# Optimization experiments

Hardware: AMD Instinct MI355X
Metric: run time of the kernel (lower is better)

The kernel has to match this reference:

```python
import math
import jax, jax.numpy as jnp
import numpy as np

NEG = -1.0e10  # matches LARGE_NUMBER padding in the original
K_SUBSET = 8
N_SAMPLES = 2


def log_conv(aL, aR, K):
    """Log-space convolution of two count distributions, truncated to counts 0..K-1.
    aL, aR: [..., K] log-values; returns c[m] = logsumexp_j aL[j] + aR[m-j]."""
    jj = jnp.arange(K)[:, None]
    mm = jnp.arange(K)[None, :]
    idx = mm - jj  # [K(j), K(m)]
    valid = idx >= 0
    aRg = aR[..., jnp.clip(idx, 0, K - 1)]  # [..., K, K]
    t = aL[..., :, None] + jnp.where(valid, aRg, NEG)
    return jax.nn.logsumexp(t, axis=-2)


def up_pass(theta, k):
    """theta: [B, N] logits (N power of two). Returns list of per-level log-ESP
    tables, levels[l]: [B, N/2^l, k+1]; levels[-1][:,0,j] = log e_j(exp theta)."""
    B, N = theta.shape
    K = k + 1
    leaf = jnp.full((B, N, K), NEG, theta.dtype)
    leaf = leaf.at[..., 0].set(0.0).at[..., 1].set(theta)
    levels = [leaf]
    a = leaf
    while a.shape[1] > 1:
        a = log_conv(a[:, 0::2], a[:, 1::2], K)
        levels.append(a)
    return levels


def down_marginals(levels, theta, k):
    """Exact inclusion marginals P(x_i=1 | sum=k) via tree forward-backward."""
    K = k + 1
    B = theta.shape[0]
    ext = jnp.full((B, 1, K), NEG, theta.dtype).at[..., 0].set(0.0)
    for lvl in range(len(levels) - 2, -1, -1):
        a = levels[lvl]
        aL, aR = a[:, 0::2], a[:, 1::2]
        extL = log_conv(ext, aR, K)  # ESP of everything outside left subtree
        extR = log_conv(ext, aL, K)
        ext = jnp.stack([extL, extR], axis=2).reshape(B, a.shape[1], K)
    logZ = levels[-1][:, 0, k]  # log e_k over all items
    # P(x_i=1) = exp(theta_i) * e_{k-1}(others) / e_k(all)
    return jnp.exp(theta + ext[..., k - 1] - logZ[:, None])


def sample_counts(levels, k, n_samples, key):
    """Top-down exact sampling of k-subsets; returns leaf counts [S, B, N] in {0,1}."""
    K = k + 1
    B = levels[0].shape[0]
    counts = jnp.full((n_samples, B, 1), k, jnp.int32)
    jj = jnp.arange(K)
    for lvl in range(len(levels) - 2, -1, -1):
        a = levels[lvl]
        aL, aR = a[:, 0::2], a[:, 1::2]
        n = aL.shape[1]
        idx = counts[..., None] - jj  # desired right-count, [S,B,n,K]
        valid = idx >= 0
        aRg = jnp.take_along_axis(
            jnp.broadcast_to(aR[None], (n_samples, B, n, K)),
            jnp.clip(idx, 0, k), axis=-1)
        logits = aL[None] + jnp.where(valid, aRg, NEG)
        key, sub = jax.random.split(key)
        g = jax.random.gumbel(sub, logits.shape, logits.dtype)
        cL = jnp.argmax(logits + g, axis=-1).astype(jnp.int32)
        cR = counts - cL
        counts = jnp.stack([cL, cR], axis=-1).reshape(n_samples, B, 2 * n)
    return counts


def setup_inputs() -> dict:
    key = jax.random.key(0)
    scores = jax.random.normal(key, (8192, 32, 8), dtype=jnp.float32)
    return {"scores": scores}


def reference(scores):
    nnodes, choices, ensemble = scores.shape
    k = min(K_SUBSET, choices)
    flat = jnp.transpose(scores, (0, 2, 1)).reshape(nnodes * ensemble, choices)
    N = 2 ** math.ceil(math.log2(choices))
    if N > choices:
        flat = jnp.concatenate(
            [flat, jnp.full((flat.shape[0], N - choices), NEG, flat.dtype)], axis=1)
    levels = up_pass(flat, k)
    marg_flat = down_marginals(levels, flat, k)[:, :choices]  # [B, choices]
    marginals = jnp.transpose(
        marg_flat.reshape(nnodes, ensemble, choices), (0, 2, 1))  # [nnodes, choices, ensemble]
    counts = sample_counts(levels, k, N_SAMPLES, jax.random.key(42))
    counts = counts[:, :, :choices].astype(scores.dtype)
    samples = jnp.transpose(
        counts.reshape(N_SAMPLES, nnodes, ensemble, choices), (0, 1, 3, 2))
    # straight-through: hard samples forward, marginal gradients backward
    samples = jax.lax.stop_gradient(samples - marginals[None]) + marginals[None]
    return samples, marginals
```

## Files before the change

### kernel.cpp

```cpp
#include <hip/hip_runtime.h>
#include <stdint.h>


__host__ __device__ __forceinline__ void tf2x32(uint32_t k0, uint32_t k1,
                                                uint32_t x0, uint32_t x1,
                                                uint32_t& y0, uint32_t& y1) {
  const uint32_t ks[3] = {k0, k1, k0 ^ k1 ^ 0x1BD11BDAu};
  x0 += ks[0]; x1 += ks[1];
  const int R0[4] = {13, 15, 26, 6};
  const int R1[4] = {17, 29, 16, 24};
#pragma unroll
  for (int i = 0; i < 5; ++i) {
    const int* R = (i & 1) ? R1 : R0;
#pragma unroll
    for (int rr = 0; rr < 4; ++rr) {
      x0 += x1;
      x1 = (x1 << R[rr]) | (x1 >> (32 - R[rr]));
      x1 ^= x0;
    }
    x0 += ks[(i + 1) % 3];
    x1 += ks[(i + 2) % 3] + (uint32_t)(i + 1);
  }
  y0 = x0; y1 = x1;
}

struct TFKeys { uint32_t v[10]; };

__device__ __forceinline__ float gumbel_draw(uint32_t sk0, uint32_t sk1,
                                             uint32_t f) {
  uint32_t y0, y1;
  tf2x32(sk0, sk1, 0u, f, y0, y1);
  uint32_t bits = y0 ^ y1;
  uint32_t fb = (bits >> 9) | 0x3f800000u;
  float u = __uint_as_float(fb) - 1.0f;
  const float tiny = 1.17549435e-38f;
  float rr = fmaxf(tiny, u + tiny);
  return -logf(-logf(rr));
}

template<bool FAST> __device__ __forceinline__ float expT(float x) {
  return FAST ? __expf(x) : expf(x);
}
template<bool FAST> __device__ __forceinline__ float logT(float x) {
  return FAST ? __logf(x) : logf(x);
}

template<int SIN, int SOUT, bool FAST>
__device__ __forceinline__ void conv_level(const float (&aL)[SIN],
                                           const float (&aR)[SIN],
                                           float (&o)[SOUT]) {
#pragma unroll
  for (int m = 1; m < SOUT; ++m) {
    const int jlo = (m - (SIN - 1) > 0) ? (m - (SIN - 1)) : 0;
    const int jhi = (m < SIN - 1) ? m : (SIN - 1);
    float t[SIN];
#pragma unroll
    for (int j = 0; j < SIN; ++j)
      if (j >= jlo && j <= jhi) t[j] = aL[j] + aR[m - j];
    float amax = t[jlo];
#pragma unroll
    for (int j = 0; j < SIN; ++j)
      if (j > jlo && j <= jhi) amax = fmaxf(amax, t[j]);
    float s = 0.0f;
#pragma unroll
    for (int j = 0; j < SIN; ++j)
      if (j >= jlo && j <= jhi) s += expT<FAST>(t[j] - amax);
    o[m] = logT<FAST>(s) + amax;
  }
}

template<int SSIB, int MLO, int MHI, bool FAST>
__device__ __forceinline__ void ext_level(const float (&ein)[8],
                                          const float* sib, float (&eo)[8]) {
#pragma unroll
  for (int m = MLO; m <= MHI; ++m) {
    const int jlo = (m - (SSIB - 1) > 0) ? (m - (SSIB - 1)) : 0;
    float t[8];
#pragma unroll
    for (int j = 0; j < 8; ++j)
      if (j >= jlo && j <= m) t[j] = ein[j] + sib[m - j];
    float amax = t[jlo];
#pragma unroll
    for (int j = 0; j < 8; ++j)
      if (j > jlo && j <= m) amax = fmaxf(amax, t[j]);
    float s = 0.0f;
#pragma unroll
    for (int j = 0; j < 8; ++j)
      if (j >= jlo && j <= m) s += expT<FAST>(t[j] - amax);
    eo[m] = logT<FAST>(s) + amax;
  }
}

#define ENT 144

__global__ __launch_bounds__(128, 2) void simple_sampler_kernel(
    const float* __restrict__ scores, float* __restrict__ out,
    int nnodes, TFKeys keys) {
  const int tid = threadIdx.x;
  const int w = tid >> 6;
  const int lane = tid & 63;
  const int p = lane & 1;
  const int r = lane >> 1;
  const int row = (blockIdx.x * 2 + w) * 32 + r;
  const int node = row >> 3, e = row & 7;
  const int B = nnodes * 8;

  __shared__ float lds[2 * ENT * 32];
  float* W = &lds[w * (ENT * 32)];
#define L(E) W[(E) * 32 + r]

  float th[16];
  const float* sc = scores + node * 256 + e + p * 128;
#pragma unroll
  for (int c = 0; c < 16; ++c) th[c] = sc[c * 8];
#pragma unroll
  for (int c = 0; c < 16; ++c) L(16 * p + c) = th[c];

  float l1r[8], th2r[8];
#pragma unroll
  for (int n1l = 0; n1l < 8; ++n1l) {
    float tL = th[2 * n1l], tR = th[2 * n1l + 1];
    float amax = fmaxf(tR, tL);
    float s = expf(tR - amax) + expf(tL - amax);
    l1r[n1l] = logf(s) + amax;
    th2r[n1l] = tL + tR;
    int n1 = 8 * p + n1l;
    L(32 + n1) = l1r[n1l];
    L(48 + n1) = th2r[n1l];
  }
  float l2r[4][5];
#pragma unroll
  for (int n2l = 0; n2l < 4; ++n2l) {
    float aL[3] = {0.0f, l1r[2 * n2l], th2r[2 * n2l]};
    float aR[3] = {0.0f, l1r[2 * n2l + 1], th2r[2 * n2l + 1]};
    float o5[5];
    conv_level<3, 5, false>(aL, aR, o5);
    l2r[n2l][0] = 0.0f;
    int n2 = 4 * p + n2l;
#pragma unroll
    for (int m = 1; m < 5; ++m) { l2r[n2l][m] = o5[m]; L(64 + n2 * 4 + m - 1) = o5[m]; }
  }
  float l3r[2][9];
#pragma unroll
  for (int n3l = 0; n3l < 2; ++n3l) {
    float o9[9];
    conv_level<5, 9, false>(l2r[2 * n3l], l2r[2 * n3l + 1], o9);
    l3r[n3l][0] = 0.0f;
    int n3 = 2 * p + n3l;
#pragma unroll
    for (int m = 1; m < 9; ++m) { l3r[n3l][m] = o9[m]; L(96 + n3 * 8 + m - 1) = o9[m]; }
  }
  {
    float o9[9];
    conv_level<9, 9, false>(l3r[0], l3r[1], o9);
#pragma unroll
    for (int m = 1; m < 9; ++m) L(128 + p * 8 + m - 1) = o9[m];
  }

  __builtin_amdgcn_wave_barrier();

  float A0[9], A1[9];
  A0[0] = 0.0f; A1[0] = 0.0f;
#pragma unroll
  for (int m = 1; m < 9; ++m) { A0[m] = L(128 + m - 1); A1[m] = L(136 + m - 1); }

  float logZ;
  {
    float t[9];
#pragma unroll
    for (int j = 0; j < 9; ++j) t[j] = A0[j] + A1[8 - j];
    float amax = t[0];
#pragma unroll
    for (int j = 1; j < 9; ++j) amax = fmaxf(amax, t[j]);
    float s = 0.0f;
#pragma unroll
    for (int j = 0; j < 9; ++j) s += __expf(t[j] - amax);
    logZ = __logf(s) + amax;
  }

  {
    float e4v[8];
    e4v[0] = 0.0f;
#pragma unroll
    for (int m = 1; m < 8; ++m) e4v[m] = p ? A0[m] : A1[m];
    float* mb = out + 2 * B * 32 + node * 256 + e;
#pragma unroll
    for (int n3l = 0; n3l < 2; ++n3l) {
      float e3[8];
      ext_level<9, 0, 7, true>(e4v, l3r[n3l ^ 1], e3);
#pragma unroll
      for (int c2 = 0; c2 < 2; ++c2) {
        const int n2l = 2 * n3l + c2;
        float e2v[8];
        ext_level<5, 4, 7, true>(e3, l2r[n2l ^ 1], e2v);
#pragma unroll
        for (int c1 = 0; c1 < 2; ++c1) {
          const int n1l = 2 * n2l + c1;
          float sib1[3] = {0.0f, l1r[n1l ^ 1], th2r[n1l ^ 1]};
          float e1m[8];
          ext_level<3, 6, 7, true>(e2v, sib1, e1m);
          const int colL = 16 * p + 2 * n1l;
          {
            float t6 = e1m[6] + th[2 * n1l + 1];
            float t7 = e1m[7];
            float amax = fmaxf(t6, t7);
            float s = __expf(t6 - amax) + __expf(t7 - amax);
            mb[colL * 8] = __expf((th[2 * n1l] + (__logf(s) + amax)) - logZ);
          }
          {
            float t6 = e1m[6] + th[2 * n1l];
            float t7 = e1m[7];
            float amax = fmaxf(t6, t7);
            float s = __expf(t6 - amax) + __expf(t7 - amax);
            mb[(colL + 1) * 8] = __expf((th[2 * n1l + 1] + (__logf(s) + amax)) - logZ);
          }
        }
      }
    }
  }

  const uint32_t t9 = (uint32_t)(p * B + row) * 9u;
  int c0, c1;
  {
    float best = 0.0f; int bj = 0;
#pragma unroll
    for (int j = 0; j < 9; ++j) {
      float g = gumbel_draw(keys.v[0], keys.v[1], t9 + (uint32_t)j);
      float v = (A0[j] + A1[8 - j]) + g;
      if (j == 0) { best = v; } else if (v > best) { best = v; bj = j; }
    }
    c0 = bj; c1 = 8 - bj;
  }
  int c1v[4];
  {
    const int n0 = c0 ? c0 + 1 : 0;
    const int n1c = c1 ? c1 + 1 : 0;
    const int tot = n0 + n1c;
    float b0 = -3.0e38f, b1 = -3.0e38f;
    int j0 = 0, j1 = 0;
    for (int t = 0; t < tot; ++t) {
      const bool is1 = (t >= n0);
      const int j = is1 ? (t - n0) : t;
      const int c = is1 ? c1 : c0;
      const int i = is1 ? 1 : 0;
      const int idx = c - j;
      float aL = (j == 0) ? 0.0f : L(96 + 16 * i + j - 1);
      float aR = (idx == 0) ? 0.0f : L(96 + 16 * i + 8 + idx - 1);
      float g = gumbel_draw(keys.v[2], keys.v[3],
                            2u * t9 + (uint32_t)(9 * i + j));
      float v = (aL + aR) + g;
      if (is1) { if (v > b1) { b1 = v; j1 = j; } }
      else     { if (v > b0) { b0 = v; j0 = j; } }
    }
    c1v[0] = j0; c1v[1] = c0 - j0; c1v[2] = j1; c1v[3] = c1 - j1;
  }
  uint32_t pk2 = 0;
  {
#pragma unroll
    for (int i = 0; i < 4; ++i) {
      int c = c1v[i];
      float best = -3.0e38f; int bj = 0;
#pragma unroll
      for (int j = 0; j < 5; ++j) {
        float g = gumbel_draw(keys.v[4], keys.v[5],
                              4u * t9 + (uint32_t)(i * 9 + j));
        int idx = c - j;
        int cl = min(max(idx, 1), 4);
        float ar = L(64 + (2 * i + 1) * 4 + cl - 1);
        float af = (idx == 0) ? 0.0f : ar;
        float aL = (j == 0) ? 0.0f : L(64 + (2 * i) * 4 + j - 1);
        float v = (aL + af) + g;
        if (idx >= 0 && idx <= 4 && v > best) { best = v; bj = j; }
      }
      pk2 |= ((uint32_t)bj << (8 * i)) | ((uint32_t)(c - bj) << (8 * i + 4));
    }
  }
  uint64_t pk64 = 0;
  {
    const uint32_t sk0 = keys.v[6], sk1 = keys.v[7];
    const uint32_t fb0 = 8u * t9;
#pragma unroll 2
    for (int i = 0; i < 8; ++i) {
      int c = (int)((pk2 >> (4 * i)) & 15u);
      float aL1 = L(32 + 2 * i), aL2 = L(48 + 2 * i);
      float arm1 = L(32 + 2 * i + 1), arm2 = L(48 + 2 * i + 1);
      uint32_t fb = fb0 + (uint32_t)(i * 9);
      float best = -3.0e38f; int bj = 0;
#pragma unroll
      for (int j = 0; j < 3; ++j) {
        float g = gumbel_draw(sk0, sk1, fb + (uint32_t)j);
        int idx = c - j;
        float af = (idx == 1) ? arm1 : ((idx == 2) ? arm2 : 0.0f);
        float aLj = (j == 0) ? 0.0f : ((j == 1) ? aL1 : aL2);
        float v = (aLj + af) + g;
        if (idx >= 0 && idx <= 2 && v > best) { best = v; bj = j; }
      }
      pk64 |= ((uint64_t)(uint32_t)bj << (8 * i)) |
              ((uint64_t)(uint32_t)(c - bj) << (8 * i + 4));
    }
  }
  {
    const uint32_t sk0 = keys.v[8], sk1 = keys.v[9];
    const uint32_t fb0 = 16u * t9;
    float* bs = out + p * (B * 32) + node * 256 + e;
    uint64_t lst = 0; int m4 = 0;
#pragma unroll
    for (int i = 0; i < 16; ++i) {
      int c = (int)((uint32_t)(pk64 >> (4 * i)) & 15u);
      if (c == 1) {
        lst |= ((uint64_t)(uint32_t)i) << (4 * m4);
        ++m4;
      } else {
        int bj = c >> 1;
        bs[16 * i] = (float)bj;
        bs[16 * i + 8] = (float)(c - bj);
      }
    }
    for (int t = 0; t < m4; ++t) {
      int i = (int)((lst >> (4 * t)) & 15u);
      float thL = L(2 * i);
      float thR = L(2 * i + 1);
      uint32_t fb = fb0 + (uint32_t)(i * 9);
      float g0 = gumbel_draw(sk0, sk1, fb);
      float g1 = gumbel_draw(sk0, sk1, fb + 1u);
      float v0 = thR + g0;
      float v1 = thL + g1;
      int bj = (v1 > v0) ? 1 : 0;
      bs[16 * i] = (float)bj;
      bs[16 * i + 8] = (float)(1 - bj);
    }
  }
#undef L
}

extern "C" void kernel_launch(void* const* d_in, const int* in_sizes, int n_in,
                              void* d_out, int out_size, void* d_ws, size_t ws_size,
                              hipStream_t stream) {
  const float* scores = (const float*)d_in[0];
  float* out = (float*)d_out;
  const int nnodes = in_sizes[0] / (32 * 8);
  const int B = nnodes * 8;

  TFKeys K;
  uint32_t k0 = 0u, k1 = 42u;
  for (int t = 0; t < 5; ++t) {
    uint32_t n0, n1, s0, s1;
    tf2x32(k0, k1, 0u, 0u, n0, n1);
    tf2x32(k0, k1, 0u, 1u, s0, s1);
    K.v[2 * t] = s0; K.v[2 * t + 1] = s1;
    k0 = n0; k1 = n1;
  }

  dim3 grid((unsigned)(B / 64)), block(128);
  hipLaunchKernelGGL(simple_sampler_kernel, grid, block, 0, stream,
                     scores, out, nnodes, K);
}
```

Before: 114.0 us.

## Split each row across four lanes to raise parallelism and occupancy

Each row is now handled by four lanes instead of two: every lane owns 8 of the 32 choices in the up pass, and the root level is spread across lanes through shared memory. The sampling descent is split by sample (p) and by half-tree (q), and the root choice is merged with a lane shuffle. Blocks grow to 256 threads with a padded shared table of stride 65, so each row gets twice the threads and fewer registers per thread. The cost is more shared-memory traffic and extra lane-to-lane exchange, and the root-level shared-memory sums use non-unrolled loops.

```diff
diff --git a/kernel.cpp b/kernel.cpp
--- a/kernel.cpp
+++ b/kernel.cpp
@@ -93,68 +93,87 @@
 
 #define ENT 144
 
-__global__ __launch_bounds__(128, 2) void simple_sampler_kernel(
+__global__ __launch_bounds__(256, 4) void simple_sampler_kernel(
     const float* __restrict__ scores, float* __restrict__ out,
     int nnodes, TFKeys keys) {
   const int tid = threadIdx.x;
   const int w = tid >> 6;
   const int lane = tid & 63;
-  const int p = lane & 1;
-  const int r = lane >> 1;
-  const int row = (blockIdx.x * 2 + w) * 32 + r;
+  const int sub = lane & 3;
+  const int q = sub & 1;
+  const int p = sub >> 1;
+  const int r = lane >> 2;
+  const int slot = w * 16 + r;
+  const int row = blockIdx.x * 64 + slot;
   const int node = row >> 3, e = row & 7;
   const int B = nnodes * 8;
-
-  __shared__ float lds[2 * ENT * 32];
-  float* W = &lds[w * (ENT * 32)];
-#define L(E) W[(E) * 32 + r]
-
-  float th[16];
-  const float* sc = scores + node * 256 + e + p * 128;
-#pragma unroll
-  for (int c = 0; c < 16; ++c) th[c] = sc[c * 8];
-#pragma unroll
-  for (int c = 0; c < 16; ++c) L(16 * p + c) = th[c];
-
-  float l1r[8], th2r[8];
-#pragma unroll
-  for (int n1l = 0; n1l < 8; ++n1l) {
-    float tL = th[2 * n1l], tR = th[2 * n1l + 1];
+  const int t = sub;
+
+  __shared__ float tab[ENT * 65];
+#define L(E) tab[(E) * 65 + slot]
+
+  float th[8];
+  const float* sc = scores + node * 256 + e + t * 64;
+#pragma unroll
+  for (int c = 0; c < 8; ++c) th[c] = sc[c * 8];
+#pragma unroll
+  for (int c = 0; c < 8; ++c) L(8 * t + c) = th[c];
+
+  float l1r[4], th2r[4];
+#pragma unroll
+  for (int i = 0; i < 4; ++i) {
+    float tL = th[2 * i], tR = th[2 * i + 1];
     float amax = fmaxf(tR, tL);
     float s = expf(tR - amax) + expf(tL - amax);
-    l1r[n1l] = logf(s) + amax;
-    th2r[n1l] = tL + tR;
-    int n1 = 8 * p + n1l;
-    L(32 + n1) = l1r[n1l];
-    L(48 + n1) = th2r[n1l];
-  }
-  float l2r[4][5];
-#pragma unroll
-  for (int n2l = 0; n2l < 4; ++n2l) {
-    float aL[3] = {0.0f, l1r[2 * n2l], th2r[2 * n2l]};
-    float aR[3] = {0.0f, l1r[2 * n2l + 1], th2r[2 * n2l + 1]};
+    l1r[i] = logf(s) + amax;
+    th2r[i] = tL + tR;
+    int n1 = 4 * t + i;
+    L(32 + n1) = l1r[i];
+    L(48 + n1) = th2r[i];
+  }
+  float l2r[2][5];
+#pragma unroll
+  for (int i = 0; i < 2; ++i) {
+    float aL[3] = {0.0f, l1r[2 * i], th2r[2 * i]};
+    float aR[3] = {0.0f, l1r[2 * i + 1], th2r[2 * i + 1]};
     float o5[5];
     conv_level<3, 5, false>(aL, aR, o5);
-    l2r[n2l][0] = 0.0f;
-    int n2 = 4 * p + n2l;
-#pragma unroll
-    for (int m = 1; m < 5; ++m) { l2r[n2l][m] = o5[m]; L(64 + n2 * 4 + m - 1) = o5[m]; }
-  }
-  float l3r[2][9];
-#pragma unroll
-  for (int n3l = 0; n3l < 2; ++n3l) {
+    l2r[i][0] = 0.0f;
+    int n2 = 2 * t + i;
+#pragma unroll
+    for (int m = 1; m < 5; ++m) { l2r[i][m] = o5[m]; L(64 + n2 * 4 + m - 1) = o5[m]; }
+  }
+  {
     float o9[9];
-    conv_level<5, 9, false>(l2r[2 * n3l], l2r[2 * n3l + 1], o9);
-    l3r[n3l][0] = 0.0f;
-    int n3 = 2 * p + n3l;
-#pragma unroll
-    for (int m = 1; m < 9; ++m) { l3r[n3l][m] = o9[m]; L(96 + n3 * 8 + m - 1) = o9[m]; }
-  }
-  {
-    float o9[9];
-    conv_level<9, 9, false>(l3r[0], l3r[1], o9);
-#pragma unroll
-    for (int m = 1; m < 9; ++m) L(128 + p * 8 + m - 1) = o9[m];
+    conv_level<5, 9, false>(l2r[0], l2r[1], o9);
+#pragma unroll
+    for (int m = 1; m < 9; ++m) L(96 + t * 8 + m - 1) = o9[m];
+  }
+
+  __builtin_amdgcn_wave_barrier();
+
+  {
+    const int eA = 96 + 16 * p;
+    const int eB = eA + 8;
+#pragma unroll
+    for (int k = 0; k < 4; ++k) {
+      int m = q ? (k + 3) : ((k < 2) ? (k + 1) : (k + 5));
+      float amax = -3.0e38f;
+      for (int j = 0; j <= m; ++j) {
+        float a = j ? L(eA + j - 1) : 0.0f;
+        int mj = m - j;
+        float b = mj ? L(eB + mj - 1) : 0.0f;
+        amax = fmaxf(amax, a + b);
+      }
+      float s = 0.0f;
+      for (int j = 0; j <= m; ++j) {
+        float a = j ? L(eA + j - 1) : 0.0f;
+        int mj = m - j;
+        float b = mj ? L(eB + mj - 1) : 0.0f;
+        s += expf((a + b) - amax);
+      }
+      L(128 + 8 * p + m - 1) = logf(s) + amax;
+    }
   }
 
   __builtin_amdgcn_wave_barrier();
@@ -166,15 +185,15 @@
 
   float logZ;
   {
-    float t[9];
-#pragma unroll
-    for (int j = 0; j < 9; ++j) t[j] = A0[j] + A1[8 - j];
-    float amax = t[0];
-#pragma unroll
-    for (int j = 1; j < 9; ++j) amax = fmaxf(amax, t[j]);
+    float tv[9];
+#pragma unroll
+    for (int j = 0; j < 9; ++j) tv[j] = A0[j] + A1[8 - j];
+    float amax = tv[0];
+#pragma unroll
+    for (int j = 1; j < 9; ++j) amax = fmaxf(amax, tv[j]);
     float s = 0.0f;
 #pragma unroll
-    for (int j = 0; j < 9; ++j) s += __expf(t[j] - amax);
+    for (int j = 0; j < 9; ++j) s += __expf(tv[j] - amax);
     logZ = __logf(s) + amax;
   }
 
@@ -183,151 +202,153 @@
     e4v[0] = 0.0f;
 #pragma unroll
     for (int m = 1; m < 8; ++m) e4v[m] = p ? A0[m] : A1[m];
+    float sib3[9];
+    sib3[0] = 0.0f;
+#pragma unroll
+    for (int m = 1; m < 9; ++m) sib3[m] = L(96 + (t ^ 1) * 8 + m - 1);
+    float e3[8];
+    ext_level<9, 0, 7, true>(e4v, sib3, e3);
     float* mb = out + 2 * B * 32 + node * 256 + e;
 #pragma unroll
-    for (int n3l = 0; n3l < 2; ++n3l) {
-      float e3[8];
-      ext_level<9, 0, 7, true>(e4v, l3r[n3l ^ 1], e3);
-#pragma unroll
-      for (int c2 = 0; c2 < 2; ++c2) {
-        const int n2l = 2 * n3l + c2;
-        float e2v[8];
-        ext_level<5, 4, 7, true>(e3, l2r[n2l ^ 1], e2v);
-#pragma unroll
-        for (int c1 = 0; c1 < 2; ++c1) {
-          const int n1l = 2 * n2l + c1;
-          float sib1[3] = {0.0f, l1r[n1l ^ 1], th2r[n1l ^ 1]};
-          float e1m[8];
-          ext_level<3, 6, 7, true>(e2v, sib1, e1m);
-          const int colL = 16 * p + 2 * n1l;
-          {
-            float t6 = e1m[6] + th[2 * n1l + 1];
-            float t7 = e1m[7];
-            float amax = fmaxf(t6, t7);
-            float s = __expf(t6 - amax) + __expf(t7 - amax);
-            mb[colL * 8] = __expf((th[2 * n1l] + (__logf(s) + amax)) - logZ);
-          }
-          {
-            float t6 = e1m[6] + th[2 * n1l];
-            float t7 = e1m[7];
-            float amax = fmaxf(t6, t7);
-            float s = __expf(t6 - amax) + __expf(t7 - amax);
-            mb[(colL + 1) * 8] = __expf((th[2 * n1l + 1] + (__logf(s) + amax)) - logZ);
-          }
+    for (int i2 = 0; i2 < 2; ++i2) {
+      float e2v[8];
+      ext_level<5, 4, 7, true>(e3, l2r[i2 ^ 1], e2v);
+#pragma unroll
+      for (int i1l = 0; i1l < 2; ++i1l) {
+        const int i1 = 2 * i2 + i1l;
+        float sib1[3] = {0.0f, l1r[i1 ^ 1], th2r[i1 ^ 1]};
+        float e1m[8];
+        ext_level<3, 6, 7, true>(e2v, sib1, e1m);
+        const int colL = 8 * t + 2 * i1;
+        {
+          float t6 = e1m[6] + th[2 * i1 + 1];
+          float t7 = e1m[7];
+          float amax = fmaxf(t6, t7);
+          float s = __expf(t6 - amax) + __expf(t7 - amax);
+          mb[colL * 8] = __expf((th[2 * i1] + (__logf(s) + amax)) - logZ);
         }
+        {
+          float t6 = e1m[6] + th[2 * i1];
+          float t7 = e1m[7];
+          float amax = fmaxf(t6, t7);
+          float s = __expf(t6 - amax) + __expf(t7 - amax);
+          mb[(colL + 1) * 8] = __expf((th[2 * i1 + 1] + (__logf(s) + amax)) - logZ);
+        }
       }
     }
   }
 
   const uint32_t t9 = (uint32_t)(p * B + row) * 9u;
-  int c0, c1;
-  {
-    float best = 0.0f; int bj = 0;
-#pragma unroll
-    for (int j = 0; j < 9; ++j) {
-      float g = gumbel_draw(keys.v[0], keys.v[1], t9 + (uint32_t)j);
-      float v = (A0[j] + A1[8 - j]) + g;
-      if (j == 0) { best = v; } else if (v > best) { best = v; bj = j; }
-    }
-    c0 = bj; c1 = 8 - bj;
-  }
-  int c1v[4];
-  {
-    const int n0 = c0 ? c0 + 1 : 0;
-    const int n1c = c1 ? c1 + 1 : 0;
-    const int tot = n0 + n1c;
-    float b0 = -3.0e38f, b1 = -3.0e38f;
-    int j0 = 0, j1 = 0;
-    for (int t = 0; t < tot; ++t) {
-      const bool is1 = (t >= n0);
-      const int j = is1 ? (t - n0) : t;
-      const int c = is1 ? c1 : c0;
-      const int i = is1 ? 1 : 0;
-      const int idx = c - j;
-      float aL = (j == 0) ? 0.0f : L(96 + 16 * i + j - 1);
-      float aR = (idx == 0) ? 0.0f : L(96 + 16 * i + 8 + idx - 1);
-      float g = gumbel_draw(keys.v[2], keys.v[3],
-                            2u * t9 + (uint32_t)(9 * i + j));
-      float v = (aL + aR) + g;
-      if (is1) { if (v > b1) { b1 = v; j1 = j; } }
-      else     { if (v > b0) { b0 = v; j0 = j; } }
-    }
-    c1v[0] = j0; c1v[1] = c0 - j0; c1v[2] = j1; c1v[3] = c1 - j1;
-  }
-  uint32_t pk2 = 0;
-  {
-#pragma unroll
-    for (int i = 0; i < 4; ++i) {
-      int c = c1v[i];
-      float best = -3.0e38f; int bj = 0;
+  int bj;
+  {
+    float vb = -3.0e38f; int jb = 0;
+    const int jbase = q * 5;
+#pragma unroll
+    for (int tci = 0; tci < 5; ++tci) {
+      int j = jbase + tci;
+      if (j <= 8) {
+        float g = gumbel_draw(keys.v[0], keys.v[1], t9 + (uint32_t)j);
+        float v = (A0[j] + A1[8 - j]) + g;
+        if (v > vb) { vb = v; jb = j; }
+      }
+    }
+    float vo = __shfl_xor(vb, 1);
+    int jo = __shfl_xor(jb, 1);
+    float vlo = q ? vo : vb; int jlo_ = q ? jo : jb;
+    float vhi = q ? vb : vo; int jhi_ = q ? jb : jo;
+    bj = (vhi > vlo) ? jhi_ : jlo_;
+  }
+  int cA, cB;
+  {
+    int c = q ? (8 - bj) : bj;
+    int bj1 = 0;
+    if (c > 0) {
+      float best = -3.0e38f;
+      const int eA = 96 + 16 * q, eB = eA + 8;
+      for (int j = 0; j <= c; ++j) {
+        float a = j ? L(eA + j - 1) : 0.0f;
+        int idx = c - j;
+        float b = idx ? L(eB + idx - 1) : 0.0f;
+        float g = gumbel_draw(keys.v[2], keys.v[3],
+                              2u * t9 + (uint32_t)(9 * q + j));
+        float v = (a + b) + g;
+        if (v > best) { best = v; bj1 = j; }
+      }
+    }
+    cA = bj1; cB = c - bj1;
+  }
+  int c2o[4];
+  {
+#pragma unroll
+    for (int k = 0; k < 2; ++k) {
+      const int i2 = 2 * q + k;
+      int c = k ? cB : cA;
+      float best = -3.0e38f; int bj2 = 0;
 #pragma unroll
       for (int j = 0; j < 5; ++j) {
         float g = gumbel_draw(keys.v[4], keys.v[5],
-                              4u * t9 + (uint32_t)(i * 9 + j));
+                              4u * t9 + (uint32_t)(i2 * 9 + j));
         int idx = c - j;
         int cl = min(max(idx, 1), 4);
-        float ar = L(64 + (2 * i + 1) * 4 + cl - 1);
-        float af = (idx == 0) ? 0.0f : ar;
-        float aL = (j == 0) ? 0.0f : L(64 + (2 * i) * 4 + j - 1);
-        float v = (aL + af) + g;
-        if (idx >= 0 && idx <= 4 && v > best) { best = v; bj = j; }
-      }
-      pk2 |= ((uint32_t)bj << (8 * i)) | ((uint32_t)(c - bj) << (8 * i + 4));
-    }
-  }
-  uint64_t pk64 = 0;
-  {
-    const uint32_t sk0 = keys.v[6], sk1 = keys.v[7];
-    const uint32_t fb0 = 8u * t9;
-#pragma unroll 2
-    for (int i = 0; i < 8; ++i) {
-      int c = (int)((pk2 >> (4 * i)) & 15u);
-      float aL1 = L(32 + 2 * i), aL2 = L(48 + 2 * i);
-      float arm1 = L(32 + 2 * i + 1), arm2 = L(48 + 2 * i + 1);
-      uint32_t fb = fb0 + (uint32_t)(i * 9);
-      float best = -3.0e38f; int bj = 0;
+        float b = L(64 + (2 * i2 + 1) * 4 + cl - 1);
+        float bf = (idx == 0) ? 0.0f : b;
+        float a = (j == 0) ? 0.0f : L(64 + (2 * i2) * 4 + j - 1);
+        float v = (a + bf) + g;
+        if (idx >= 0 && idx <= 4 && v > best) { best = v; bj2 = j; }
+      }
+      c2o[2 * k] = bj2; c2o[2 * k + 1] = c - bj2;
+    }
+  }
+  int c3o[8];
+  {
+#pragma unroll
+    for (int k = 0; k < 4; ++k) {
+      const int i3 = 4 * q + k;
+      int c = c2o[k];
+      float aL1 = L(32 + 2 * i3), aL2 = L(48 + 2 * i3);
+      float bR1 = L(32 + 2 * i3 + 1), bR2 = L(48 + 2 * i3 + 1);
+      float best = -3.0e38f; int bj3 = 0;
 #pragma unroll
       for (int j = 0; j < 3; ++j) {
-        float g = gumbel_draw(sk0, sk1, fb + (uint32_t)j);
+        float g = gumbel_draw(keys.v[6], keys.v[7],
+                              8u * t9 + (uint32_t)(i3 * 9 + j));
         int idx = c - j;
-        float af = (idx == 1) ? arm1 : ((idx == 2) ? arm2 : 0.0f);
-        float aLj = (j == 0) ? 0.0f : ((j == 1) ? aL1 : aL2);
-        float v = (aLj + af) + g;
-        if (idx >= 0 && idx <= 2 && v > best) { best = v; bj = j; }
-      }
-      pk64 |= ((uint64_t)(uint32_t)bj << (8 * i)) |
-              ((uint64_t)(uint32_t)(c - bj) << (8 * i + 4));
+        float bf = (idx == 1) ? bR1 : ((idx == 2) ? bR2 : 0.0f);
+        float af = (j == 0) ? 0.0f : ((j == 1) ? aL1 : aL2);
+        float v = (af + bf) + g;
+        if (idx >= 0 && idx <= 2 && v > best) { best = v; bj3 = j; }
+      }
+      c3o[2 * k] = bj3; c3o[2 * k + 1] = c - bj3;
     }
   }
   {
     const uint32_t sk0 = keys.v[8], sk1 = keys.v[9];
-    const uint32_t fb0 = 16u * t9;
     float* bs = out + p * (B * 32) + node * 256 + e;
-    uint64_t lst = 0; int m4 = 0;
-#pragma unroll
-    for (int i = 0; i < 16; ++i) {
-      int c = (int)((uint32_t)(pk64 >> (4 * i)) & 15u);
+    uint32_t lst = 0; int m4 = 0;
+#pragma unroll
+    for (int k = 0; k < 8; ++k) {
+      const int i4 = 8 * q + k;
+      int c = c3o[k];
       if (c == 1) {
-        lst |= ((uint64_t)(uint32_t)i) << (4 * m4);
+        lst |= ((uint32_t)k) << (4 * m4);
         ++m4;
       } else {
-        int bj = c >> 1;
-        bs[16 * i] = (float)bj;
-        bs[16 * i + 8] = (float)(c - bj);
-      }
-    }
-    for (int t = 0; t < m4; ++t) {
-      int i = (int)((lst >> (4 * t)) & 15u);
-      float thL = L(2 * i);
-      float thR = L(2 * i + 1);
-      uint32_t fb = fb0 + (uint32_t)(i * 9);
+        int bj4 = c >> 1;
+        bs[(2 * i4) * 8] = (float)bj4;
+        bs[(2 * i4 + 1) * 8] = (float)(c - bj4);
+      }
+    }
+    for (int tt = 0; tt < m4; ++tt) {
+      int k = (int)((lst >> (4 * tt)) & 15u);
+      const int i4 = 8 * q + k;
+      float thL = L(2 * i4);
+      float thR = L(2 * i4 + 1);
+      uint32_t fb = 16u * t9 + (uint32_t)(i4 * 9);
       float g0 = gumbel_draw(sk0, sk1, fb);
       float g1 = gumbel_draw(sk0, sk1, fb + 1u);
-      float v0 = thR + g0;
-      float v1 = thL + g1;
-      int bj = (v1 > v0) ? 1 : 0;
-      bs[16 * i] = (float)bj;
-      bs[16 * i + 8] = (float)(1 - bj);
+      int bj4 = ((thL + g1) > (thR + g0)) ? 1 : 0;
+      bs[(2 * i4) * 8] = (float)bj4;
+      bs[(2 * i4 + 1) * 8] = (float)(1 - bj4);
     }
   }
 #undef L
@@ -351,7 +372,7 @@
     k0 = n0; k1 = n1;
   }
 
-  dim3 grid((unsigned)(B / 64)), block(128);
+  dim3 grid((unsigned)(B / 64)), block(256);
   hipLaunchKernelGGL(simple_sampler_kernel, grid, block, 0, stream,
                      scores, out, nnodes, K);
 }
```

After: 116.5 us. 1.02x slower.

## Compact sampling loops to valid candidates, shuffle root table, shrink blocks to one wave

Applied to the files above, without the earlier changes.

Rewrites the level-2 and level-1 sampling stages as flattened loops that visit only valid split candidates, so Gumbel draws (Threefry hashes) for impossible splits are skipped. The top-count entry of each convolution is computed directly as a sum. The root table is exchanged between lane pairs with a shuffle instead of a round trip through shared memory. Blocks shrink to a single 64-thread wave with a smaller shared-memory table. The cost is data-dependent loop trip counts, extra bit-packing arithmetic, and possible divergence across lanes.

```diff
diff --git a/kernel.cpp b/kernel.cpp
--- a/kernel.cpp
+++ b/kernel.cpp
@@ -45,12 +45,13 @@
   return FAST ? __logf(x) : logf(x);
 }
 
-template<int SIN, int SOUT, bool FAST>
+template<int SIN, int SOUT, bool FAST, bool LS>
 __device__ __forceinline__ void conv_level(const float (&aL)[SIN],
                                            const float (&aR)[SIN],
                                            float (&o)[SOUT]) {
 #pragma unroll
   for (int m = 1; m < SOUT; ++m) {
+    if (LS && m == SOUT - 1) { o[m] = aL[SIN - 1] + aR[SIN - 1]; continue; }
     const int jlo = (m - (SIN - 1) > 0) ? (m - (SIN - 1)) : 0;
     const int jhi = (m < SIN - 1) ? m : (SIN - 1);
     float t[SIN];
@@ -91,23 +92,20 @@
   }
 }
 
-#define ENT 144
-
-__global__ __launch_bounds__(128, 2) void simple_sampler_kernel(
+#define ENT 128
+
+__global__ __launch_bounds__(64, 2) void simple_sampler_kernel(
     const float* __restrict__ scores, float* __restrict__ out,
     int nnodes, TFKeys keys) {
-  const int tid = threadIdx.x;
-  const int w = tid >> 6;
-  const int lane = tid & 63;
+  const int lane = threadIdx.x;
   const int p = lane & 1;
   const int r = lane >> 1;
-  const int row = (blockIdx.x * 2 + w) * 32 + r;
+  const int row = blockIdx.x * 32 + r;
   const int node = row >> 3, e = row & 7;
   const int B = nnodes * 8;
 
-  __shared__ float lds[2 * ENT * 32];
-  float* W = &lds[w * (ENT * 32)];
-#define L(E) W[(E) * 32 + r]
+  __shared__ float tab[ENT * 32];
+#define L(E) tab[(E) * 32 + r]
 
   float th[16];
   const float* sc = scores + node * 256 + e + p * 128;
@@ -134,7 +132,7 @@
     float aL[3] = {0.0f, l1r[2 * n2l], th2r[2 * n2l]};
     float aR[3] = {0.0f, l1r[2 * n2l + 1], th2r[2 * n2l + 1]};
     float o5[5];
-    conv_level<3, 5, false>(aL, aR, o5);
+    conv_level<3, 5, false, true>(aL, aR, o5);
     l2r[n2l][0] = 0.0f;
     int n2 = 4 * p + n2l;
 #pragma unroll
@@ -144,37 +142,40 @@
 #pragma unroll
   for (int n3l = 0; n3l < 2; ++n3l) {
     float o9[9];
-    conv_level<5, 9, false>(l2r[2 * n3l], l2r[2 * n3l + 1], o9);
+    conv_level<5, 9, false, true>(l2r[2 * n3l], l2r[2 * n3l + 1], o9);
     l3r[n3l][0] = 0.0f;
     int n3 = 2 * p + n3l;
 #pragma unroll
     for (int m = 1; m < 9; ++m) { l3r[n3l][m] = o9[m]; L(96 + n3 * 8 + m - 1) = o9[m]; }
   }
-  {
-    float o9[9];
-    conv_level<9, 9, false>(l3r[0], l3r[1], o9);
-#pragma unroll
-    for (int m = 1; m < 9; ++m) L(128 + p * 8 + m - 1) = o9[m];
-  }
 
   __builtin_amdgcn_wave_barrier();
 
   float A0[9], A1[9];
-  A0[0] = 0.0f; A1[0] = 0.0f;
-#pragma unroll
-  for (int m = 1; m < 9; ++m) { A0[m] = L(128 + m - 1); A1[m] = L(136 + m - 1); }
+  {
+    float l4o[9];
+    conv_level<9, 9, false, false>(l3r[0], l3r[1], l4o);
+    A0[0] = 0.0f; A1[0] = 0.0f;
+#pragma unroll
+    for (int m = 1; m < 9; ++m) {
+      float own = l4o[m];
+      float oth = __shfl_xor(own, 1);
+      A0[m] = p ? oth : own;
+      A1[m] = p ? own : oth;
+    }
+  }
 
   float logZ;
   {
-    float t[9];
-#pragma unroll
-    for (int j = 0; j < 9; ++j) t[j] = A0[j] + A1[8 - j];
-    float amax = t[0];
-#pragma unroll
-    for (int j = 1; j < 9; ++j) amax = fmaxf(amax, t[j]);
+    float tv[9];
+#pragma unroll
+    for (int j = 0; j < 9; ++j) tv[j] = A0[j] + A1[8 - j];
+    float amax = tv[0];
+#pragma unroll
+    for (int j = 1; j < 9; ++j) amax = fmaxf(amax, tv[j]);
     float s = 0.0f;
 #pragma unroll
-    for (int j = 0; j < 9; ++j) s += __expf(t[j] - amax);
+    for (int j = 0; j < 9; ++j) s += __expf(tv[j] - amax);
     logZ = __logf(s) + amax;
   }
 
@@ -194,8 +195,8 @@
         float e2v[8];
         ext_level<5, 4, 7, true>(e3, l2r[n2l ^ 1], e2v);
 #pragma unroll
-        for (int c1 = 0; c1 < 2; ++c1) {
-          const int n1l = 2 * n2l + c1;
+        for (int c1i = 0; c1i < 2; ++c1i) {
+          const int n1l = 2 * n2l + c1i;
           float sib1[3] = {0.0f, l1r[n1l ^ 1], th2r[n1l ^ 1]};
           float e1m[8];
           ext_level<3, 6, 7, true>(e2v, sib1, e1m);
@@ -244,60 +245,106 @@
       const int c = is1 ? c1 : c0;
       const int i = is1 ? 1 : 0;
       const int idx = c - j;
-      float aL = (j == 0) ? 0.0f : L(96 + 16 * i + j - 1);
-      float aR = (idx == 0) ? 0.0f : L(96 + 16 * i + 8 + idx - 1);
+      float a = (j == 0) ? 0.0f : L(96 + 16 * i + j - 1);
+      float b = (idx == 0) ? 0.0f : L(96 + 16 * i + 8 + idx - 1);
       float g = gumbel_draw(keys.v[2], keys.v[3],
                             2u * t9 + (uint32_t)(9 * i + j));
-      float v = (aL + aR) + g;
+      float v = (a + b) + g;
       if (is1) { if (v > b1) { b1 = v; j1 = j; } }
       else     { if (v > b0) { b0 = v; j0 = j; } }
     }
     c1v[0] = j0; c1v[1] = c0 - j0; c1v[2] = j1; c1v[3] = c1 - j1;
   }
-  uint32_t pk2 = 0;
-  {
+  uint32_t c3Pk = 0;
+  {
+    int nA[4], jl4[4];
 #pragma unroll
     for (int i = 0; i < 4; ++i) {
       int c = c1v[i];
-      float best = -3.0e38f; int bj = 0;
-#pragma unroll
-      for (int j = 0; j < 5; ++j) {
-        float g = gumbel_draw(keys.v[4], keys.v[5],
-                              4u * t9 + (uint32_t)(i * 9 + j));
-        int idx = c - j;
-        int cl = min(max(idx, 1), 4);
-        float ar = L(64 + (2 * i + 1) * 4 + cl - 1);
-        float af = (idx == 0) ? 0.0f : ar;
-        float aL = (j == 0) ? 0.0f : L(64 + (2 * i) * 4 + j - 1);
-        float v = (aL + af) + g;
-        if (idx >= 0 && idx <= 4 && v > best) { best = v; bj = j; }
-      }
-      pk2 |= ((uint32_t)bj << (8 * i)) | ((uint32_t)(c - bj) << (8 * i + 4));
-    }
+      int lo = (c - 4 > 0) ? (c - 4) : 0;
+      int hi = (c < 4) ? c : 4;
+      jl4[i] = lo;
+      nA[i] = c ? (hi - lo + 1) : 0;
+    }
+    const int s1 = nA[0], s2 = s1 + nA[1], s3 = s2 + nA[2];
+    const int T = s3 + nA[3];
+    const uint32_t sPk = ((uint32_t)s1 << 8) | ((uint32_t)s2 << 16) |
+                         ((uint32_t)s3 << 24);
+    const uint32_t jloPk = (uint32_t)jl4[0] | ((uint32_t)jl4[1] << 4) |
+                           ((uint32_t)jl4[2] << 8) | ((uint32_t)jl4[3] << 12);
+    const uint32_t cPk = (uint32_t)c1v[0] | ((uint32_t)c1v[1] << 8) |
+                         ((uint32_t)c1v[2] << 16) | ((uint32_t)c1v[3] << 24);
+    int curI = 0, bj = 0;
+    float best = -3.0e38f;
+    for (int t = 0; t < T; ++t) {
+      int i = (int)(t >= s1) + (int)(t >= s2) + (int)(t >= s3);
+      bool nw = (i != curI);
+      int cP = (int)((cPk >> (8 * curI)) & 255u);
+      uint32_t fl = ((uint32_t)bj << (8 * curI)) |
+                    ((uint32_t)(cP - bj) << (8 * curI + 4));
+      c3Pk |= nw ? fl : 0u;
+      best = nw ? -3.0e38f : best;
+      bj = nw ? 0 : bj;
+      curI = i;
+      int base = (int)((sPk >> (8 * i)) & 255u);
+      int c = (int)((cPk >> (8 * i)) & 255u);
+      int j = (int)((jloPk >> (4 * i)) & 15u) + (t - base);
+      int idx = c - j;
+      float a = j ? L(64 + 8 * i + j - 1) : 0.0f;
+      float b = idx ? L(64 + 8 * i + 4 + idx - 1) : 0.0f;
+      float g = gumbel_draw(keys.v[4], keys.v[5],
+                            4u * t9 + (uint32_t)(9 * i + j));
+      float v = (a + b) + g;
+      if (v > best) { best = v; bj = j; }
+    }
+    int cP = (int)((cPk >> (8 * curI)) & 255u);
+    c3Pk |= ((uint32_t)bj << (8 * curI)) |
+            ((uint32_t)(cP - bj) << (8 * curI + 4));
   }
   uint64_t pk64 = 0;
   {
-    const uint32_t sk0 = keys.v[6], sk1 = keys.v[7];
-    const uint32_t fb0 = 8u * t9;
-#pragma unroll 2
-    for (int i = 0; i < 8; ++i) {
-      int c = (int)((pk2 >> (4 * i)) & 15u);
-      float aL1 = L(32 + 2 * i), aL2 = L(48 + 2 * i);
-      float arm1 = L(32 + 2 * i + 1), arm2 = L(48 + 2 * i + 1);
-      uint32_t fb = fb0 + (uint32_t)(i * 9);
-      float best = -3.0e38f; int bj = 0;
-#pragma unroll
-      for (int j = 0; j < 3; ++j) {
-        float g = gumbel_draw(sk0, sk1, fb + (uint32_t)j);
-        int idx = c - j;
-        float af = (idx == 1) ? arm1 : ((idx == 2) ? arm2 : 0.0f);
-        float aLj = (j == 0) ? 0.0f : ((j == 1) ? aL1 : aL2);
-        float v = (aLj + af) + g;
-        if (idx >= 0 && idx <= 2 && v > best) { best = v; bj = j; }
-      }
-      pk64 |= ((uint64_t)(uint32_t)bj << (8 * i)) |
-              ((uint64_t)(uint32_t)(c - bj) << (8 * i + 4));
-    }
+    uint64_t sPk = 0;
+    uint32_t jloPk = 0;
+    int run = 0;
+#pragma unroll
+    for (int k = 0; k < 8; ++k) {
+      int c = (int)((c3Pk >> (4 * k)) & 15u);
+      int lo = (c - 2 > 0) ? (c - 2) : 0;
+      int hi = (c < 2) ? c : 2;
+      jloPk |= (uint32_t)lo << (4 * k);
+      sPk |= (uint64_t)(uint32_t)run << (8 * k);
+      run += c ? (hi - lo + 1) : 0;
+    }
+    const int T = run;
+    int curI = 0, bj = 0;
+    float best = -3.0e38f;
+    for (int t = 0; t < T; ++t) {
+      int i = 0;
+#pragma unroll
+      for (int k = 1; k < 8; ++k)
+        i += (int)(t >= (int)((sPk >> (8 * k)) & 255u));
+      bool nw = (i != curI);
+      int cP = (int)((c3Pk >> (4 * curI)) & 15u);
+      uint64_t fl = ((uint64_t)(uint32_t)bj << (8 * curI)) |
+                    ((uint64_t)(uint32_t)(cP - bj) << (8 * curI + 4));
+      pk64 |= nw ? fl : (uint64_t)0;
+      best = nw ? -3.0e38f : best;
+      bj = nw ? 0 : bj;
+      curI = i;
+      int base = (int)((sPk >> (8 * i)) & 255u);
+      int c = (int)((c3Pk >> (4 * i)) & 15u);
+      int j = (int)((jloPk >> (4 * i)) & 15u) + (t - base);
+      int idx = c - j;
+      float a = j ? L(32 + ((j - 1) << 4) + 2 * i) : 0.0f;
+      float b = idx ? L(32 + ((idx - 1) << 4) + 2 * i + 1) : 0.0f;
+      float g = gumbel_draw(keys.v[6], keys.v[7],
+                            8u * t9 + (uint32_t)(9 * i + j));
+      float v = (a + b) + g;
+      if (v > best) { best = v; bj = j; }
+    }
+    int cP = (int)((c3Pk >> (4 * curI)) & 15u);
+    pk64 |= ((uint64_t)(uint32_t)bj << (8 * curI)) |
+            ((uint64_t)(uint32_t)(cP - bj) << (8 * curI + 4));
   }
   {
     const uint32_t sk0 = keys.v[8], sk1 = keys.v[9];
@@ -316,16 +363,14 @@
         bs[16 * i + 8] = (float)(c - bj);
       }
     }
-    for (int t = 0; t < m4; ++t) {
-      int i = (int)((lst >> (4 * t)) & 15u);
+    for (int tt = 0; tt < m4; ++tt) {
+      int i = (int)((lst >> (4 * tt)) & 15u);
       float thL = L(2 * i);
       float thR = L(2 * i + 1);
       uint32_t fb = fb0 + (uint32_t)(i * 9);
       float g0 = gumbel_draw(sk0, sk1, fb);
       float g1 = gumbel_draw(sk0, sk1, fb + 1u);
-      float v0 = thR + g0;
-      float v1 = thL + g1;
-      int bj = (v1 > v0) ? 1 : 0;
+      int bj = ((thL + g1) > (thR + g0)) ? 1 : 0;
       bs[16 * i] = (float)bj;
       bs[16 * i + 8] = (float)(1 - bj);
     }
@@ -351,7 +396,7 @@
     k0 = n0; k1 = n1;
   }
 
-  dim3 grid((unsigned)(B / 64)), block(128);
+  dim3 grid((unsigned)(B / 32)), block(64);
   hipLaunchKernelGGL(simple_sampler_kernel, grid, block, 0, stream,
                      scores, out, nnodes, K);
 }
```

Measured after the change: 117.2 us. 1.03x slower.
